# Kernel tuning notes

Measured on AMD Instinct MI355X. Metric: run time of the kernel, lower is better.

The kernel has to match this reference:

```python
import jax, jax.numpy as jnp
import numpy as np

NEG = -1e30   # log-space 'zero' (safe under fp32 exp underflow)
EPS = 1e-7    # keras.backend.epsilon()


def _ctc_loss(logprobs, labels):
    """CTC negative log-likelihood, blank = C-1 (tf.nn.ctc_loss / ctc_batch_cost).

    logprobs: [B, T, C] log probabilities; labels: [B, L] ints in [0, C-1).
    Full input_length=T and label_length=L (as forced by CTCLayer).
    Returns [B, 1] loss, matching ctc_batch_cost's expand_dims.
    """
    B, T, C = logprobs.shape
    L = labels.shape[1]
    blank = C - 1
    S = 2 * L + 1  # extended label sequence: blank, l1, blank, ..., lL, blank

    ext = jnp.full((B, S), blank, dtype=labels.dtype).at[:, 1::2].set(labels)
    # transition s-2 -> s allowed iff z_s != blank and z_s != z_{s-2}
    skip = jnp.zeros((B, S), dtype=bool).at[:, 2:].set(ext[:, 2:] != ext[:, :-2])
    skip = skip & (ext != blank)

    # per-frame logprob of each extended-label symbol: [B, T, S]
    lp_ext = jnp.take_along_axis(logprobs, ext[:, None, :], axis=2)

    init = (jnp.full((B, S), NEG, logprobs.dtype)
            .at[:, 0].set(lp_ext[:, 0, 0])
            .at[:, 1].set(lp_ext[:, 0, 1]))
    pad1 = jnp.full((B, 1), NEG, logprobs.dtype)
    pad2 = jnp.full((B, 2), NEG, logprobs.dtype)

    def step(alpha, lp_t):
        s1 = jnp.concatenate([pad1, alpha[:, :-1]], axis=1)
        s2 = jnp.where(skip, jnp.concatenate([pad2, alpha[:, :-2]], axis=1), NEG)
        m = jnp.maximum(jnp.maximum(alpha, s1), s2)
        new = lp_t + m + jnp.log(jnp.exp(alpha - m) + jnp.exp(s1 - m) + jnp.exp(s2 - m))
        return new, None

    alpha_T, _ = jax.lax.scan(step, init, jnp.swapaxes(lp_ext, 0, 1)[1:])  # scan over T-1 frames
    return -jnp.logaddexp(alpha_T[:, -1], alpha_T[:, -2])[:, None]


def setup_inputs() -> dict:
    key = jax.random.key(0)
    k1, k2 = jax.random.split(key)
    B, T, C, L = 256, 1024, 256, 128
    y_pred = jax.random.uniform(k1, (B, T, C), dtype=jnp.float32)  # softmax-like probs
    y_true = jax.random.randint(k2, (B, L), 0, C - 1, dtype=jnp.int32)  # blank=C-1 excluded
    return {"y_true": y_true, "y_pred": y_pred}


def reference(y_true, y_pred):
    # ctc_batch_cost: logits = log(y_pred + epsilon), blank index = num_classes - 1,
    # input_length = T and label_length = L for every batch element (per CTCLayer.call).
    logprobs = jnp.log(y_pred + EPS)
    loss = _ctc_loss(logprobs, y_true)  # [B, 1]
    return loss
```

## Files before the change

### kernel.cpp

```cpp
#include <hip/hip_runtime.h>


#define T_DIM 1024
#define C_DIM 256
#define L_DIM 128
#define DPF   16
#define EPSF  1e-7f
#define LN2D  0.69314718055994530942

__device__ __forceinline__ double dpp_shr1_f64(double old, double v) {
    int rlo = __builtin_amdgcn_update_dpp(__double2loint(old), __double2loint(v),
                                          0x138 , 0xF, 0xF, false);
    int rhi = __builtin_amdgcn_update_dpp(__double2hiint(old), __double2hiint(v),
                                          0x138 , 0xF, 0xF, false);
    return __hiloint2double(rhi, rlo);
}

__device__ __forceinline__ int wave_imax_all(int v) {
#define STAGE(CTRL) { int t_ = __builtin_amdgcn_update_dpp(v, v, CTRL, 0xF, 0xF, false); \
                      v = v > t_ ? v : t_; }
    STAGE(0x111)
    STAGE(0x112)
    STAGE(0x114)
    STAGE(0x118)
    STAGE(0x142)
    STAGE(0x143)
#undef STAGE
    return __builtin_amdgcn_readlane(v, 63);
}

__device__ __forceinline__ void ctc_step(double p0, double p1, double pB,
                                         double k1, double k3, double& a0,
                                         double& r1, double& r2, double& r3, double& r4) {
    double sA4 = dpp_shr1_f64(a0,  r4);
    double sA3 = dpp_shr1_f64(0.0, r3);
    double n1 = p0 * fma(k1, sA3, r1 + sA4);
    double n2 = pB * (r2 + r1);
    double n3 = p1 * fma(k3, r1, r3 + r2);
    double n4 = pB * (r4 + r3);
    a0 *= pB;
    r1 = n1; r2 = n2; r3 = n3; r4 = n4;
}

__global__ __launch_bounds__(64, 1)
void ctc_fwd(const int* __restrict__ labels, const float* __restrict__ ypred,
             float* __restrict__ out) {
    const int b = blockIdx.x;
    const int l = threadIdx.x;
    const float* Yb = ypred + (size_t)b * (T_DIM * C_DIM);

    const int2 lab = ((const int2*)(labels + b * L_DIM))[l];
    const int c0 = lab.x, c1 = lab.y;
    int cB;
    asm("v_mov_b32 %0, 255" : "=v"(cB));

    const int labprev = __shfl_up(c1, 1, 64);
    const double k1 = (l == 0 || labprev == c0) ? 0.0 : 1.0;
    const double k3 = (c1 == c0) ? 0.0 : 1.0;

    double a0 = (double)(Yb[cB] + EPSF);
    double r1 = (l == 0) ? (double)(Yb[c0] + EPSF) : 0.0;
    double r2 = 0.0, r3 = 0.0, r4 = 0.0;
    int e2acc = 0;

    float f0[DPF], f1[DPF], fB[DPF];
#pragma unroll
    for (int d = 0; d < DPF; ++d) {
        const float* p = Yb + (size_t)(1 + d) * C_DIM;
        f0[d] = p[c0]; f1[d] = p[c1]; fB[d] = p[cB];
    }

    for (int tb = 1; tb <= 993; tb += 16) {
#pragma unroll
        for (int d = 0; d < 16; ++d) {
            ctc_step((double)(f0[d] + EPSF), (double)(f1[d] + EPSF),
                     (double)(fB[d] + EPSF), k1, k3, a0, r1, r2, r3, r4);
            int tn = tb + d + DPF;
            tn = tn > T_DIM - 1 ? T_DIM - 1 : tn;
            const float* p = Yb + (size_t)tn * C_DIM;
            f0[d] = p[c0]; f1[d] = p[c1]; fB[d] = p[cB];
        }
        int h = __double2hiint(r1);
        int t_;
        t_ = __double2hiint(r2); h = h > t_ ? h : t_;
        t_ = __double2hiint(r3); h = h > t_ ? h : t_;
        t_ = __double2hiint(r4); h = h > t_ ? h : t_;
        t_ = __double2hiint(a0); h = h > t_ ? h : t_;
        int H = wave_imax_all(h);
        int k = (H >> 20) - 1023;
        double s = __hiloint2double((1023 - k) << 20, 0);
        r1 *= s; r2 *= s; r3 *= s; r4 *= s; a0 *= s;
        e2acc += k;
    }
#pragma unroll
    for (int d = 0; d < 15; ++d)
        ctc_step((double)(f0[d] + EPSF), (double)(f1[d] + EPSF),
                 (double)(fB[d] + EPSF), k1, k3, a0, r1, r2, r3, r4);

    if (l == 63) {
        double sum = r3 + r4;
        int hi = __double2hiint(sum), lo = __double2loint(sum);
        int e = (hi >> 20) - 1023;
        double mant = __hiloint2double((hi & 0x000FFFFF) | (1023 << 20), lo);
        double lg2 = (double)__log2f((float)mant) + (double)(e + e2acc);
        out[b] = (float)(-LN2D * lg2);
    }
}

extern "C" void kernel_launch(void* const* d_in, const int* in_sizes, int n_in,
                              void* d_out, int out_size, void* d_ws, size_t ws_size,
                              hipStream_t stream) {
    const int* y_true = (const int*)d_in[0];
    const float* y_pred = (const float*)d_in[1];
    float* out = (float*)d_out;
    ctc_fwd<<<256, 64, 0, stream>>>(y_true, y_pred, out);
}
```

Baseline: 364.4 us.

## Stage frame rows through an LDS ring buffer with coalesced float4 loads

Replaces the three scattered per-lane global gathers per time step with one coalesced float4 load per lane of the whole 256-class row. Rows are held in a register ring, written into an 8-slot shared-memory ring a few steps ahead, and gathered from LDS two steps ahead of use. The aim is to cut global memory transactions and hide load latency behind the serial recurrence. In exchange it adds LDS traffic and relies on single-wave in-order LDS semantics, with no barrier between the writes and the reads.

```diff
diff --git a/kernel.cpp b/kernel.cpp
--- a/kernel.cpp
+++ b/kernel.cpp
@@ -4,9 +4,12 @@
 #define T_DIM 1024
 #define C_DIM 256
 #define L_DIM 128
-#define DPF   16
 #define EPSF  1e-7f
 #define LN2D  0.69314718055994530942
+#define DG    8
+#define DL    3
+#define DS    2
+#define NS    8
 
 __device__ __forceinline__ double dpp_shr1_f64(double old, double v) {
     int rlo = __builtin_amdgcn_update_dpp(__double2loint(old), __double2loint(v),
@@ -49,6 +52,8 @@
     const int l = threadIdx.x;
     const float* Yb = ypred + (size_t)b * (T_DIM * C_DIM);
 
+    __shared__ float smem[NS * C_DIM];
+
     const int2 lab = ((const int2*)(labels + b * L_DIM))[l];
     const int c0 = lab.x, c1 = lab.y;
     int cB;
@@ -63,22 +68,41 @@
     double r2 = 0.0, r3 = 0.0, r4 = 0.0;
     int e2acc = 0;
 
-    float f0[DPF], f1[DPF], fB[DPF];
+    float4 rbuf[DG];
+    float fr0[4], fr1[4], frB[4];
+
 #pragma unroll
-    for (int d = 0; d < DPF; ++d) {
-        const float* p = Yb + (size_t)(1 + d) * C_DIM;
-        f0[d] = p[c0]; f1[d] = p[c1]; fB[d] = p[cB];
+    for (int g = DL + 1; g <= DL + DG; ++g)
+        rbuf[g & 7] = ((const float4*)(Yb + (size_t)g * C_DIM))[l];
+#pragma unroll
+    for (int w = 1; w <= DL; ++w) {
+        float4 v = ((const float4*)(Yb + (size_t)w * C_DIM))[l];
+        ((float4*)(smem + (w & 7) * C_DIM))[l] = v;
+    }
+#pragma unroll
+    for (int r = 1; r <= DS; ++r) {
+        const float* row = smem + (r & 7) * C_DIM;
+        fr0[r & 3] = row[c0]; fr1[r & 3] = row[c1]; frB[r & 3] = row[255];
     }
 
     for (int tb = 1; tb <= 993; tb += 16) {
 #pragma unroll
         for (int d = 0; d < 16; ++d) {
-            ctc_step((double)(f0[d] + EPSF), (double)(f1[d] + EPSF),
-                     (double)(fB[d] + EPSF), k1, k3, a0, r1, r2, r3, r4);
-            int tn = tb + d + DPF;
-            tn = tn > T_DIM - 1 ? T_DIM - 1 : tn;
-            const float* p = Yb + (size_t)tn * C_DIM;
-            f0[d] = p[c0]; f1[d] = p[c1]; fB[d] = p[cB];
+            const int t = tb + d;
+            {
+                const float* row = smem + ((t + DS) & 7) * C_DIM;
+                fr0[(t + DS) & 3] = row[c0];
+                fr1[(t + DS) & 3] = row[c1];
+                frB[(t + DS) & 3] = row[255];
+            }
+            {
+                const int ws = (t + DL) & 7;
+                ((float4*)(smem + ws * C_DIM))[l] = rbuf[ws];
+                int g = t + DL + DG; g = g > T_DIM - 1 ? T_DIM - 1 : g;
+                rbuf[ws] = ((const float4*)(Yb + (size_t)g * C_DIM))[l];
+            }
+            ctc_step((double)(fr0[t & 3] + EPSF), (double)(fr1[t & 3] + EPSF),
+                     (double)(frB[t & 3] + EPSF), k1, k3, a0, r1, r2, r3, r4);
         }
         int h = __double2hiint(r1);
         int t_;
@@ -92,10 +116,24 @@
         r1 *= s; r2 *= s; r3 *= s; r4 *= s; a0 *= s;
         e2acc += k;
     }
+
 #pragma unroll
-    for (int d = 0; d < 15; ++d)
-        ctc_step((double)(f0[d] + EPSF), (double)(f1[d] + EPSF),
-                 (double)(fB[d] + EPSF), k1, k3, a0, r1, r2, r3, r4);
+    for (int t = 1009; t <= 1023; ++t) {
+        {
+            const float* row = smem + ((t + DS) & 7) * C_DIM;
+            fr0[(t + DS) & 3] = row[c0];
+            fr1[(t + DS) & 3] = row[c1];
+            frB[(t + DS) & 3] = row[255];
+        }
+        {
+            const int ws = (t + DL) & 7;
+            ((float4*)(smem + ws * C_DIM))[l] = rbuf[ws];
+            int g = t + DL + DG; g = g > T_DIM - 1 ? T_DIM - 1 : g;
+            rbuf[ws] = ((const float4*)(Yb + (size_t)g * C_DIM))[l];
+        }
+        ctc_step((double)(fr0[t & 3] + EPSF), (double)(fr1[t & 3] + EPSF),
+                 (double)(frB[t & 3] + EPSF), k1, k3, a0, r1, r2, r3, r4);
+    }
 
     if (l == 63) {
         double sum = r3 + r4;
```

Measured after the change: 506.1 us. 1.39x slower.

## Stream y_pred rows into double-buffered LDS via global_load_lds for CTC recurrence

Applied to the files above, without the earlier changes.

Replaces per-lane scattered global gathers of three class probabilities per frame with coalesced whole-row async global-to-LDS copies of 16 frames at a time, double-buffered, followed by small LDS gathers with a two-frame register lookahead. The goal is to cut global-memory latency and uncoalesced gather traffic on the serial critical path of the recurrence. In exchange it moves every full row (all 256 classes) instead of only the needed entries, and adds LDS traffic and vmcnt waits each block of 16 frames.

```diff
diff --git a/kernel.cpp b/kernel.cpp
--- a/kernel.cpp
+++ b/kernel.cpp
@@ -4,9 +4,17 @@
 #define T_DIM 1024
 #define C_DIM 256
 #define L_DIM 128
-#define DPF   16
 #define EPSF  1e-7f
 #define LN2D  0.69314718055994530942
+
+typedef const __attribute__((address_space(1))) void* as1_cvp;
+typedef __attribute__((address_space(3))) void* as3_vp;
+
+__device__ __forceinline__ void gload_lds_row(const float* grow, int lane,
+                                              float* ldsrow) {
+    __builtin_amdgcn_global_load_lds((as1_cvp)(grow + 4 * lane),
+                                     (as3_vp)ldsrow, 16, 0, 0);
+}
 
 __device__ __forceinline__ double dpp_shr1_f64(double old, double v) {
     int rlo = __builtin_amdgcn_update_dpp(__double2loint(old), __double2loint(v),
@@ -42,12 +50,24 @@
     r1 = n1; r2 = n2; r3 = n3; r4 = n4;
 }
 
+#define DS_READ_ROW(rowptr) do {                                   \
+        fr0[(t + 2) & 3] = (rowptr)[c0];                           \
+        fr1[(t + 2) & 3] = (rowptr)[c1];                           \
+        frB[(t + 2) & 3] = (rowptr)[255];                          \
+    } while (0)
+
+#define DO_STEP()                                                             \
+    ctc_step((double)(fr0[t & 3] + EPSF), (double)(fr1[t & 3] + EPSF),        \
+             (double)(frB[t & 3] + EPSF), k1, k3, a0, r1, r2, r3, r4)
+
 __global__ __launch_bounds__(64, 1)
 void ctc_fwd(const int* __restrict__ labels, const float* __restrict__ ypred,
              float* __restrict__ out) {
     const int b = blockIdx.x;
     const int l = threadIdx.x;
     const float* Yb = ypred + (size_t)b * (T_DIM * C_DIM);
+
+    __shared__ float smem[2 * 16 * C_DIM];
 
     const int2 lab = ((const int2*)(labels + b * L_DIM))[l];
     const int c0 = lab.x, c1 = lab.y;
@@ -63,22 +83,45 @@
     double r2 = 0.0, r3 = 0.0, r4 = 0.0;
     int e2acc = 0;
 
-    float f0[DPF], f1[DPF], fB[DPF];
+    float fr0[4], fr1[4], frB[4];
+
 #pragma unroll
-    for (int d = 0; d < DPF; ++d) {
-        const float* p = Yb + (size_t)(1 + d) * C_DIM;
-        f0[d] = p[c0]; f1[d] = p[c1]; fB[d] = p[cB];
+    for (int j = 0; j < 16; ++j)
+        gload_lds_row(Yb + (size_t)(1 + j) * C_DIM, l, smem + j * C_DIM);
+    asm volatile("s_waitcnt vmcnt(0)" ::: "memory");
+#pragma unroll
+    for (int r = 1; r <= 2; ++r) {
+        const float* row = smem + (r - 1) * C_DIM;
+        fr0[r & 3] = row[c0]; fr1[r & 3] = row[c1]; frB[r & 3] = row[255];
     }
 
-    for (int tb = 1; tb <= 993; tb += 16) {
+    for (int k = 0; k < 63; ++k) {
+        {
+            const int g0 = 17 + 16 * k;
+            float* dst = smem + ((k + 1) & 1) * (16 * C_DIM);
 #pragma unroll
-        for (int d = 0; d < 16; ++d) {
-            ctc_step((double)(f0[d] + EPSF), (double)(f1[d] + EPSF),
-                     (double)(fB[d] + EPSF), k1, k3, a0, r1, r2, r3, r4);
-            int tn = tb + d + DPF;
-            tn = tn > T_DIM - 1 ? T_DIM - 1 : tn;
-            const float* p = Yb + (size_t)tn * C_DIM;
-            f0[d] = p[c0]; f1[d] = p[c1]; fB[d] = p[cB];
+            for (int j = 0; j < 16; ++j) {
+                int g = g0 + j; g = g > T_DIM - 1 ? T_DIM - 1 : g;
+                gload_lds_row(Yb + (size_t)g * C_DIM, l, dst + j * C_DIM);
+            }
+        }
+        const int tb = 1 + 16 * k;
+        const float* bufk = smem + (k & 1) * (16 * C_DIM);
+        const float* bufn = smem + ((k + 1) & 1) * (16 * C_DIM);
+#pragma unroll
+        for (int d = 0; d < 14; ++d) {
+            const int t = tb + d;
+            const float* row = bufk + ((2 + d) & 15) * C_DIM;
+            DS_READ_ROW(row);
+            DO_STEP();
+        }
+        asm volatile("s_waitcnt vmcnt(0)" ::: "memory");
+#pragma unroll
+        for (int d = 14; d < 16; ++d) {
+            const int t = tb + d;
+            const float* row = bufn + ((2 + d) & 15) * C_DIM;
+            DS_READ_ROW(row);
+            DO_STEP();
         }
         int h = __double2hiint(r1);
         int t_;
@@ -87,15 +130,22 @@
         t_ = __double2hiint(r4); h = h > t_ ? h : t_;
         t_ = __double2hiint(a0); h = h > t_ ? h : t_;
         int H = wave_imax_all(h);
-        int k = (H >> 20) - 1023;
-        double s = __hiloint2double((1023 - k) << 20, 0);
+        int kk = (H >> 20) - 1023;
+        double s = __hiloint2double((1023 - kk) << 20, 0);
         r1 *= s; r2 *= s; r3 *= s; r4 *= s; a0 *= s;
-        e2acc += k;
+        e2acc += kk;
     }
+
+    {
+        const float* buft = smem + (63 & 1) * (16 * C_DIM);
 #pragma unroll
-    for (int d = 0; d < 15; ++d)
-        ctc_step((double)(f0[d] + EPSF), (double)(f1[d] + EPSF),
-                 (double)(fB[d] + EPSF), k1, k3, a0, r1, r2, r3, r4);
+        for (int t = 1009; t <= 1023; ++t) {
+            int rr = t + 2; rr = rr > T_DIM - 1 ? T_DIM - 1 : rr;
+            const float* row = buft + ((rr - 1) & 15) * C_DIM;
+            DS_READ_ROW(row);
+            DO_STEP();
+        }
+    }
 
     if (l == 63) {
         double sum = r3 + r4;
```

After: 368.0 us. Within noise of the previous version (+1.0%).
